# Kernel optimization log

Measured on AMD Instinct MI355X. Metric: run time of the kernel, lower is better.

## Reference

```python
import jax, jax.numpy as jnp
import numpy as np

B, S0, S1 = 4, 768, 256
T = S0 + S1
W0, W1 = 2048, 1024
N, K, H = 8, 1, 256  # num_heads, num_kv_heads (MQA), head_dim
G = N // K
MAX_WAVELENGTH = 10000.0
BIG_NEG = -2.3819763e+38


def _apply_rope(x, positions):
    """RoPE: positions [B,L] applied to x [B,L,heads,H]."""
    half = x.shape[-1] // 2
    freq_exponents = (2.0 / x.shape[-1]) * jnp.arange(half, dtype=jnp.float32)
    timescale = MAX_WAVELENGTH ** freq_exponents  # [half]
    radians = positions[..., None].astype(jnp.float32) / timescale  # [B,L,half]
    radians = radians[..., None, :]  # [B,L,1,half]
    sin, cos = jnp.sin(radians), jnp.cos(radians)
    x1, x2 = jnp.split(x.astype(jnp.float32), 2, axis=-1)
    res = jnp.concatenate([x1 * cos - x2 * sin, x2 * cos + x1 * sin], axis=-1)
    return res.astype(x.dtype)


def setup_inputs() -> dict:
    key = jax.random.key(0)
    ks = jax.random.split(key, 8)
    x0 = jax.random.normal(ks[0], (B, S0, W0), dtype=jnp.float32)
    x1 = jax.random.normal(ks[1], (B, S1, W1), dtype=jnp.float32)
    positions = jnp.broadcast_to(jnp.arange(T, dtype=jnp.int32)[None, :], (B, T))
    # causal mask [B,1,T,T]
    attn_mask = jnp.broadcast_to(jnp.tril(jnp.ones((T, T), dtype=bool))[None, None], (B, 1, T, T))
    # lecun_normal on the width (in) axis
    q0_w = jax.random.normal(ks[2], (N, W0, H), dtype=jnp.float32) / np.sqrt(W0)
    kv0_w = jax.random.normal(ks[3], (2, K, W0, H), dtype=jnp.float32) / np.sqrt(W0)
    out0_w = jax.random.normal(ks[4], (N, H, W0), dtype=jnp.float32) / np.sqrt(N * H)
    q1_w = jax.random.normal(ks[5], (N, W1, H), dtype=jnp.float32) / np.sqrt(W1)
    kv1_w = jax.random.normal(ks[6], (2, K, W1, H), dtype=jnp.float32) / np.sqrt(W1)
    out1_w = jax.random.normal(ks[7], (N, H, W1), dtype=jnp.float32) / np.sqrt(N * H)
    return {"x0": x0, "x1": x1, "positions": positions, "attn_mask": attn_mask,
            "q0_w": q0_w, "kv0_w": kv0_w, "out0_w": out0_w,
            "q1_w": q1_w, "kv1_w": kv1_w, "out1_w": out1_w}


def reference(x0, x1, positions, attn_mask, q0_w, kv0_w, out0_w, q1_w, kv1_w, out1_w):
    dtype = x0.dtype
    # per-modality QKV projections (num_kv_heads != num_heads branch)
    q0 = jnp.einsum('BTD,NDH->BTNH', x0, q0_w.astype(dtype))
    k0, v0 = jnp.einsum('BSD,2KDH->2BSKH', x0, kv0_w.astype(dtype))
    q1 = jnp.einsum('BTD,NDH->BTNH', x1, q1_w.astype(dtype))
    k1, v1 = jnp.einsum('BSD,2KDH->2BSKH', x1, kv1_w.astype(dtype))
    q = jnp.concatenate([q0, q1], axis=1)  # [B,T,N,H]
    k = jnp.concatenate([k0, k1], axis=1)  # [B,T,K,H]
    v = jnp.concatenate([v0, v1], axis=1)
    q = _apply_rope(q, positions) * (H ** -0.5)
    k = _apply_rope(k, positions)
    # prefill cache init: cache_size == attn_mask.shape[-1] == T, so no padding
    idx = jnp.full((B,), T, dtype=jnp.int32)
    # GQA attention
    qg = q.reshape(B, T, K, G, H)  # 'B T (K G) H -> B T K G H'
    logits = jnp.einsum('BTKGH,BSKH->BKGTS', qg, k, preferred_element_type=jnp.float32)
    masked = jnp.where(attn_mask[:, :, None, :, :], logits, BIG_NEG)
    probs = jax.nn.softmax(masked, axis=-1).astype(dtype)
    enc = jnp.einsum('BKGTS,BSKH->BTKGH', probs, v).reshape(B, T, N, H)
    out0 = jnp.einsum('BTNH,NHD->BTD', enc[:, :S0], out0_w.astype(dtype))
    out1 = jnp.einsum('BTNH,NHD->BTD', enc[:, S0:], out1_w.astype(dtype))
    return (out0, out1, idx, k, v)
```

## Files before the change

kernel.cpp:

```cpp
#include <hip/hip_runtime.h>

typedef unsigned short u16;
typedef __attribute__((ext_vector_type(8))) short short8;
typedef __attribute__((ext_vector_type(4))) float f32x4;
typedef __attribute__((ext_vector_type(4))) unsigned short u16x4;

__device__ __forceinline__ u16 f2bf(float f){
  unsigned u = __float_as_uint(f);
  u += 0x7FFFu + ((u >> 16) & 1u);
  return (u16)(u >> 16);
}
__device__ __forceinline__ float bf2f(u16 h){
  return __uint_as_float(((unsigned)h) << 16);
}
__device__ __forceinline__ void gload16(const void* g, void* l){
  __builtin_amdgcn_global_load_lds((const __attribute__((address_space(1))) void*)g,
                                   (__attribute__((address_space(3))) void*)l, 16, 0, 0);
}
__device__ __forceinline__ f32x4 mfma16(short8 a, short8 b, f32x4 c){
  return __builtin_amdgcn_mfma_f32_16x16x32_bf16(a, b, c, 0, 0, 0);
}
__device__ __forceinline__ short8 ld8(const u16* p){
  return *reinterpret_cast<const short8*>(p);
}

template<int CTRL>
__device__ __forceinline__ float dppf(float x){
  return __int_as_float(__builtin_amdgcn_update_dpp(0, __float_as_int(x), CTRL, 0xF, 0xF, true));
}
__device__ __forceinline__ float rmax16(float x){
  x = fmaxf(x, dppf<0xB1>(x));
  x = fmaxf(x, dppf<0x4E>(x));
  x = fmaxf(x, dppf<0x124>(x));
  x = fmaxf(x, dppf<0x128>(x));
  return x;
}
__device__ __forceinline__ float rsum16(float x){
  x += dppf<0xB1>(x);
  x += dppf<0x4E>(x);
  x += dppf<0x124>(x);
  x += dppf<0x128>(x);
  return x;
}

__global__ void cvt_all(const float* __restrict__ x0, const float* __restrict__ x1,
                        u16* __restrict__ x0b, u16* __restrict__ x1b){
  int bid = blockIdx.x;
  const float* s; u16* d; int i;
  if (bid < 6144){ s = x0; d = x0b; i = bid * 256 + threadIdx.x; }
  else           { s = x1; d = x1b; i = (bid - 6144) * 256 + threadIdx.x; }
  float4 v = reinterpret_cast<const float4*>(s)[i];
  u16x4 o = { f2bf(v.x), f2bf(v.y), f2bf(v.z), f2bf(v.w) };
  reinterpret_cast<u16x4*>(d)[i] = o;
}

__device__ __forceinline__
void transp_body(const float* __restrict__ S, u16* __restrict__ D,
                 int K, int C, int kb, int cb){
  __shared__ float t[32][33];
  int tx = threadIdx.x & 31, ty = threadIdx.x >> 5;
  #pragma unroll
  for (int i = ty; i < 32; i += 8)
    t[i][tx] = S[(size_t)(kb + i) * C + cb + tx];
  __syncthreads();
  #pragma unroll
  for (int i = ty; i < 32; i += 8)
    D[(size_t)(cb + i) * K + kb + tx] = f2bf(t[tx][i]);
}
__global__ __launch_bounds__(256)
void transpose_all(const float* q0_w, const float* kv0_w, const float* q1_w,
                   const float* kv1_w, const float* o0_w, const float* o1_w,
                   u16* qkv0T, u16* qkv1T, u16* o0T, u16* o1T){
  int bid = blockIdx.x;
  const float* S; u16* D; int K, C, nkc, lid;
  if (bid < 4096){
    S = q0_w; D = qkv0T; K = 2048; C = 256; lid = bid;
  } else if (bid < 5120){
    S = kv0_w; D = qkv0T + (size_t)2048*2048; K = 2048; C = 256; lid = bid - 4096;
  } else if (bid < 7168){
    S = q1_w; D = qkv1T; K = 1024; C = 256; lid = bid - 5120;
  } else if (bid < 7680){
    S = kv1_w; D = qkv1T + (size_t)2048*1024; K = 1024; C = 256; lid = bid - 7168;
  } else if (bid < 11776){
    S = o0_w; D = o0T; K = 2048; C = 2048; lid = bid - 7680;
  } else {
    S = o1_w; D = o1T; K = 2048; C = 1024; lid = bid - 11776;
  }
  nkc = (K >> 5) * (C >> 5);
  int z   = lid / nkc;
  int rem = lid - z * nkc;
  int kb  = (rem / (C >> 5)) << 5;
  int cb  = (rem % (C >> 5)) << 5;
  transp_body(S + (size_t)z * K * C, D + (size_t)z * K * C, K, C, kb, cb);
}

__device__ __forceinline__
void gemm_body(const u16* __restrict__ A, int lda, int aS, int aT, int aOff,
               const u16* __restrict__ BT, int ldbt,
               u16* __restrict__ Cb, float* __restrict__ Cf, int ldc,
               int cS, int cT, int cOff, int N, int Kd, int bid, char* smem){
  int ntx = N >> 7;
  int bm = bid / ntx;
  int bn = bid - bm * ntx;
  int row0 = bm << 7, col0 = bn << 7;
  size_t arow0 = (size_t)(row0 / aS) * aT + (row0 % aS) + aOff;
  size_t crow0 = (size_t)(row0 / cS) * cT + (row0 % cS) + cOff;
  const u16* Abase = A + arow0 * (size_t)lda;
  const u16* Bbase = BT + (size_t)col0 * ldbt;
  int tid = threadIdx.x;
  int w = tid >> 6, l = tid & 63;
  int wr = (w >> 1) << 6, wc = (w & 1) << 6;
  int lr = l & 15, g4 = l >> 4, lq = (l >> 4) << 2;
  int keyr = lr & 7;
  f32x4 acc[4][4];
  #pragma unroll
  for (int m = 0; m < 4; m++)
    #pragma unroll
    for (int n = 0; n < 4; n++)
      acc[m][n] = (f32x4){0.f, 0.f, 0.f, 0.f};
  int scol = (((tid & 7) ^ ((tid >> 3) & 7)) << 3);
  const u16* gA = Abase + (size_t)(tid >> 3) * lda + scol;
  const u16* gB = Bbase + (size_t)(tid >> 3) * ldbt + scol;
  int dsto = tid * 16;

  auto STAGE = [&](char* dst, int k0){
    gload16(gA + k0,                      dst + dsto);
    gload16(gA + (size_t)32*lda  + k0,    dst + 4096  + dsto);
    gload16(gA + (size_t)64*lda  + k0,    dst + 8192  + dsto);
    gload16(gA + (size_t)96*lda  + k0,    dst + 12288 + dsto);
    gload16(gB + k0,                      dst + 16384 + dsto);
    gload16(gB + (size_t)32*ldbt + k0,    dst + 20480 + dsto);
    gload16(gB + (size_t)64*ldbt + k0,    dst + 24576 + dsto);
    gload16(gB + (size_t)96*ldbt + k0,    dst + 28672 + dsto);
  };

  STAGE(smem, 0);
  int cur = 0;
  for (int k0 = 0; k0 < Kd; k0 += 64, cur ^= 1){
    asm volatile("" ::: "memory");
    __builtin_amdgcn_s_barrier();
    asm volatile("" ::: "memory");
    if (k0 + 64 < Kd){
      STAGE(smem + (cur ^ 1) * 32768, k0 + 64);
      asm volatile("s_waitcnt vmcnt(8)" ::: "memory");
    } else {
      asm volatile("s_waitcnt vmcnt(0)" ::: "memory");
    }
    __builtin_amdgcn_s_barrier();
    asm volatile("" ::: "memory");
    const u16* As = (const u16*)(smem + cur * 32768);
    const u16* Bs = As + 8192;
    #pragma unroll
    for (int kk = 0; kk < 2; kk++){
      int so = ((g4 + kk*4) ^ keyr) << 3;
      short8 af[4], bfr[4];
      #pragma unroll
      for (int m = 0; m < 4; m++)
        af[m] = ld8(&As[(wr + m*16 + lr)*64 + so]);
      #pragma unroll
      for (int n = 0; n < 4; n++)
        bfr[n] = ld8(&Bs[(wc + n*16 + lr)*64 + so]);
      #pragma unroll
      for (int m = 0; m < 4; m++)
        #pragma unroll
        for (int n = 0; n < 4; n++)
          acc[m][n] = mfma16(af[m], bfr[n], acc[m][n]);
    }
  }
  #pragma unroll
  for (int m = 0; m < 4; m++){
    #pragma unroll
    for (int i = 0; i < 4; i++){
      size_t r = crow0 + wr + m*16 + lq + i;
      if (Cb){
        #pragma unroll
        for (int n = 0; n < 4; n++)
          Cb[r*ldc + col0 + wc + n*16 + lr] = f2bf(acc[m][n][i]);
      } else {
        #pragma unroll
        for (int n = 0; n < 4; n++)
          Cf[r*ldc + col0 + wc + n*16 + lr] = acc[m][n][i];
      }
    }
  }
}

__global__ __launch_bounds__(256)
void gemm_qkv(const u16* __restrict__ x0b, const u16* __restrict__ qkv0T,
              const u16* __restrict__ x1b, const u16* __restrict__ qkv1T,
              u16* __restrict__ qkvb){
  extern __shared__ __align__(16) char smem[];
  int bid = blockIdx.x;
  if (bid < 480)
    gemm_body(x0b, 2048, 3072, 3072, 0, qkv0T, 2048,
              qkvb, nullptr, 2560, 768, 1024, 0, 2560, 2048, bid, smem);
  else
    gemm_body(x1b, 1024, 1024, 1024, 0, qkv1T, 1024,
              qkvb, nullptr, 2560, 256, 1024, 768, 2560, 1024, bid - 480, smem);
}

__global__ __launch_bounds__(256)
void gemm_out(const u16* __restrict__ encb, const u16* __restrict__ o0T,
              const u16* __restrict__ o1T, float* __restrict__ out0,
              float* __restrict__ out1){
  extern __shared__ __align__(16) char smem[];
  int bid = blockIdx.x;
  if (bid < 384)
    gemm_body(encb, 2048, 768, 1024, 0, o0T, 2048,
              nullptr, out0, 2048, 3072, 3072, 0, 2048, 2048, bid, smem);
  else
    gemm_body(encb, 2048, 256, 1024, 768, o1T, 2048,
              nullptr, out1, 1024, 1024, 1024, 0, 1024, 2048, bid - 384, smem);
}

__global__ void rope_kernel(u16* __restrict__ qkv, const int* __restrict__ positions,
                            float* __restrict__ k_out, float* __restrict__ v_out,
                            float* __restrict__ idx_out){
  int bt = blockIdx.x;
  int j = threadIdx.x;
  float pos = (float)positions[bt];
  float ts = powf(10000.0f, (float)j * 0.0078125f);
  float rad = pos / ts;
  float sn, cs;
  sincosf(rad, &sn, &cs);
  u16* q = qkv + (size_t)bt * 2560;
  #pragma unroll
  for (int n = 0; n < 8; n++){
    float x1 = bf2f(q[n*256 + j]);
    float x2 = bf2f(q[n*256 + 128 + j]);
    q[n*256 + j]       = f2bf((x1*cs - x2*sn) * 0.0625f);
    q[n*256 + 128 + j] = f2bf((x2*cs + x1*sn) * 0.0625f);
  }
  u16* kv = q + 2048;
  float x1 = bf2f(kv[j]), x2 = bf2f(kv[128 + j]);
  float k1 = x1*cs - x2*sn, k2 = x2*cs + x1*sn;
  kv[j] = f2bf(k1); kv[128 + j] = f2bf(k2);
  size_t ko = (size_t)bt * 256;
  k_out[ko + j] = k1;  k_out[ko + 128 + j] = k2;
  v_out[ko + j] = bf2f(kv[256 + j]);
  v_out[ko + 128 + j] = bf2f(kv[384 + j]);
  if (bt == 0 && j < 4) idx_out[j] = 1024.0f;
}

__global__ void transpose_v(const u16* __restrict__ qkv, u16* __restrict__ vT){
  __shared__ u16 t[32][33];
  int b = blockIdx.z;
  int tb = blockIdx.x * 32, hb = blockIdx.y * 32;
  int tx = threadIdx.x, ty = threadIdx.y;
  #pragma unroll
  for (int i = ty; i < 32; i += 8)
    t[i][tx] = qkv[(size_t)(b*1024 + tb + i)*2560 + 2304 + hb + tx];
  __syncthreads();
  #pragma unroll
  for (int i = ty; i < 32; i += 8)
    vT[(size_t)(b*256 + hb + i)*1024 + tb + tx] = t[tx][i];
}

__global__ __launch_bounds__(256, 2)
void attn_kernel(const u16* __restrict__ qkv, const u16* __restrict__ vT,
                 u16* __restrict__ enc){
  extern __shared__ __align__(16) char smem[];
  int bid = blockIdx.x;
  int b   = bid & 3;
  int h2  = (bid >> 2) & 1;
  int qt  = 63 - (bid >> 3);
  int tid = threadIdx.x;
  int w = tid >> 6;
  int head = h2*4 + w;
  int l = tid & 63;
  int lr = l & 15;
  int g4 = l >> 4;
  int lkqe  = g4 << 3;
  int lkq16 = g4 << 4;
  int lq = g4 << 2;
  int q0 = qt << 4, nkv = q0 + 16;
  int swk = (lr & 7) << 4;
  int swv = ((lr >> 1) & 3) << 4;
  int swp = ((lr >> 2) & 3) << 4;

  const char* kbase = (const char*)qkv + (size_t)b*5242880 + 4096;
  const char* vbase = (const char*)vT + (size_t)b*524288;
  const char* ksrc[4]; const char* vsrc[4];
  int kldo[4], vldo[4];
  #pragma unroll
  for (int r = 0; r < 4; r++){
    int o = r*4096 + tid*16;
    int krow = o >> 9;
    int kcol = (o & 511) ^ ((krow & 7) << 4);
    ksrc[r] = kbase + (size_t)krow*5120 + kcol;
    kldo[r] = o;
    int vrow = o >> 6;
    int vcol = (o & 63) ^ (((vrow >> 1) & 3) << 4);
    vsrc[r] = vbase + (size_t)vrow*2048 + vcol;
    vldo[r] = 16384 + o;
  }

  const u16* qb = qkv + ((size_t)(b*1024 + q0)) * 2560 + head*256;
  short8 qf[8];
  #pragma unroll
  for (int hf = 0; hf < 8; hf++)
    qf[hf] = ld8(qb + (size_t)lr*2560 + hf*32 + lkqe);

  f32x4 o_[16];
  #pragma unroll
  for (int hf = 0; hf < 16; hf++)
    o_[hf] = (f32x4){0.f,0.f,0.f,0.f};
  float mrow[4], lrow[4];
  #pragma unroll
  for (int i = 0; i < 4; i++){ mrow[i] = -3.0e38f; lrow[i] = 0.f; }
  u16* P = (u16*)(smem + 65536 + w*1024);

  auto STAGE = [&](int buf, int kt){
    char* dst = smem + buf*32768;
    #pragma unroll
    for (int r = 0; r < 4; r++)
      gload16(ksrc[r] + (size_t)kt*5120, dst + kldo[r]);
    #pragma unroll
    for (int r = 0; r < 4; r++)
      gload16(vsrc[r] + (size_t)kt*2, dst + vldo[r]);
  };

  STAGE(0, 0);
  int cur = 0;
  for (int kt = 0; kt < nkv; kt += 32, cur ^= 1){
    asm volatile("" ::: "memory");
    __builtin_amdgcn_s_barrier();
    asm volatile("" ::: "memory");
    if (kt + 32 < nkv){
      STAGE(cur ^ 1, kt + 32);
      asm volatile("s_waitcnt vmcnt(8)" ::: "memory");
    } else {
      asm volatile("s_waitcnt vmcnt(0)" ::: "memory");
    }
    __builtin_amdgcn_s_barrier();
    asm volatile("" ::: "memory");

    const char* Kb = smem + cur*32768;
    const char* Vb = Kb + 16384;
    f32x4 s[2];
    s[0] = (f32x4){0.f,0.f,0.f,0.f};
    s[1] = (f32x4){0.f,0.f,0.f,0.f};
    #pragma unroll
    for (int hf = 0; hf < 8; hf++){
      int colb = (hf*64 + lkq16) ^ swk;
      short8 k0 = *(const short8*)(Kb + (size_t)(lr     )*512 + colb);
      short8 k1 = *(const short8*)(Kb + (size_t)(lr + 16)*512 + colb);
      s[0] = mfma16(qf[hf], k0, s[0]);
      s[1] = mfma16(qf[hf], k1, s[1]);
    }
    if (kt + 32 > q0){
      #pragma unroll
      for (int cf = 0; cf < 2; cf++)
        #pragma unroll
        for (int i = 0; i < 4; i++){
          int row_g = q0 + lq + i;
          int col_g = kt + cf*16 + lr;
          if (col_g > row_g) s[cf][i] = -1.0e30f;
        }
    }
    float mx[4];
    #pragma unroll
    for (int i = 0; i < 4; i++)
      mx[i] = rmax16(fmaxf(s[0][i], s[1][i]));
    bool nd = false;
    #pragma unroll
    for (int i = 0; i < 4; i++)
      nd = nd || (mx[i] > mrow[i] + 8.f);
    if (__ballot(nd)){
      #pragma unroll
      for (int i = 0; i < 4; i++){
        float mn = fmaxf(mrow[i], mx[i]);
        float corr = __expf(mrow[i] - mn);
        mrow[i] = mn;
        lrow[i] *= corr;
        #pragma unroll
        for (int hf = 0; hf < 16; hf++)
          o_[hf][i] *= corr;
      }
    }
    #pragma unroll
    for (int i = 0; i < 4; i++){
      float m = mrow[i];
      float p0 = __expf(s[0][i] - m);
      float p1 = __expf(s[1][i] - m);
      s[0][i] = p0; s[1][i] = p1;
      lrow[i] += rsum16(p0 + p1);
    }
    asm volatile("s_waitcnt lgkmcnt(0)" ::: "memory");
    __builtin_amdgcn_sched_barrier(0);
    #pragma unroll
    for (int cf = 0; cf < 2; cf++)
      #pragma unroll
      for (int i = 0; i < 4; i++){
        int row = lq + i;
        int by = ((row*32 + cf*16 + lr) << 1) ^ (((row >> 2) & 3) << 4);
        *(u16*)((char*)P + by) = f2bf(s[cf][i]);
      }
    asm volatile("s_waitcnt lgkmcnt(0)" ::: "memory");
    __builtin_amdgcn_sched_barrier(0);
    short8 pa;
    {
      int by = ((lr*32 + lkqe) << 1) ^ swp;
      pa = *(const short8*)((const char*)P + by);
    }
    __builtin_amdgcn_sched_barrier(0);
    #pragma unroll
    for (int hf = 0; hf < 16; hf++){
      const char* vr = Vb + (size_t)(hf*16 + lr)*64;
      short8 v0 = *(const short8*)(vr + (lkq16 ^ swv));
      o_[hf] = mfma16(pa, v0, o_[hf]);
    }
  }
  u16* eb = enc + ((size_t)(b*1024 + q0)) * 2048 + head*256;
  float inv[4];
  #pragma unroll
  for (int i = 0; i < 4; i++)
    inv[i] = 1.0f / lrow[i];
  #pragma unroll
  for (int hf = 0; hf < 16; hf++)
    #pragma unroll
    for (int i = 0; i < 4; i++)
      eb[(size_t)(lq + i)*2048 + hf*16 + lr] = f2bf(o_[hf][i] * inv[i]);
}

extern "C" void kernel_launch(void* const* d_in, const int* in_sizes, int n_in,
                              void* d_out, int out_size, void* d_ws, size_t ws_size,
                              hipStream_t stream){
  const float* x0     = (const float*)d_in[0];
  const float* x1     = (const float*)d_in[1];
  const int*   pos    = (const int*)d_in[2];
  const float* q0_w   = (const float*)d_in[4];
  const float* kv0_w  = (const float*)d_in[5];
  const float* out0_w = (const float*)d_in[6];
  const float* q1_w   = (const float*)d_in[7];
  const float* kv1_w  = (const float*)d_in[8];
  const float* out1_w = (const float*)d_in[9];

  float* out  = (float*)d_out;
  float* out0 = out;
  float* out1 = out + 6291456;
  float* idxp = out + 7340032;
  float* kout = out + 7340036;
  float* vout = out + 8388612;

  char* ws = (char*)d_ws;
  size_t off = 0;
  auto alloc = [&](size_t bytes){
    void* p = ws + off;
    off = (off + bytes + 255) & ~(size_t)255;
    return p;
  };
  u16* x0b   = (u16*)alloc((size_t)6291456 * 2);
  u16* x1b   = (u16*)alloc((size_t)1048576 * 2);
  u16* qkv0T = (u16*)alloc((size_t)2560 * 2048 * 2);
  u16* qkv1T = (u16*)alloc((size_t)2560 * 1024 * 2);
  u16* o0T   = (u16*)alloc((size_t)2048 * 2048 * 2);
  u16* o1T   = (u16*)alloc((size_t)1024 * 2048 * 2);
  u16* qkvb  = (u16*)alloc((size_t)4096 * 2560 * 2);
  u16* vTb   = (u16*)alloc((size_t)4 * 256 * 1024 * 2);
  u16* encb  = (u16*)alloc((size_t)4096 * 2048 * 2);

  hipFuncSetAttribute((const void*)attn_kernel,
                      hipFuncAttributeMaxDynamicSharedMemorySize, 69632);
  hipFuncSetAttribute((const void*)gemm_qkv,
                      hipFuncAttributeMaxDynamicSharedMemorySize, 65536);
  hipFuncSetAttribute((const void*)gemm_out,
                      hipFuncAttributeMaxDynamicSharedMemorySize, 65536);

  cvt_all<<<7168, 256, 0, stream>>>(x0, x1, x0b, x1b);
  transpose_all<<<13824, 256, 0, stream>>>(q0_w, kv0_w, q1_w, kv1_w, out0_w, out1_w,
                                           qkv0T, qkv1T, o0T, o1T);

  gemm_qkv<<<640, 256, 65536, stream>>>(x0b, qkv0T, x1b, qkv1T, qkvb);

  rope_kernel<<<4096, 128, 0, stream>>>(qkvb, pos, kout, vout, idxp);
  transpose_v<<<dim3(32, 8, 4), dim3(32,8), 0, stream>>>(qkvb, vTb);
  attn_kernel<<<512, 256, 69632, stream>>>(qkvb, vTb, encb);

  gemm_out<<<448, 256, 65536, stream>>>(encb, o0T, o1T, out0, out1);
}
```

Measured before the change: 168.6 us.

## Transpose attention MFMA operands to keep P in registers and skip LDS

Swaps the A/B operands of the QK^T and PV MFMAs so each lane holds one query row's scores. Softmax reductions then shrink to two cross-lane shuffles instead of DPP row reductions. The P tile is packed to bf16 with v_cvt_pk and rearranged into the PV operand layout through lane shuffles, so the LDS round-trip and its waits go away and the LDS allocation shrinks. The MFMA sections are also wrapped in s_setprio, and output stores become 8-byte vector writes. The risk is extra shuffle and select work, plus getting the register permutation exactly right.

```diff
diff --git a/kernel.cpp b/kernel.cpp
--- a/kernel.cpp
+++ b/kernel.cpp
@@ -23,24 +23,10 @@
 __device__ __forceinline__ short8 ld8(const u16* p){
   return *reinterpret_cast<const short8*>(p);
 }
-
-template<int CTRL>
-__device__ __forceinline__ float dppf(float x){
-  return __int_as_float(__builtin_amdgcn_update_dpp(0, __float_as_int(x), CTRL, 0xF, 0xF, true));
-}
-__device__ __forceinline__ float rmax16(float x){
-  x = fmaxf(x, dppf<0xB1>(x));
-  x = fmaxf(x, dppf<0x4E>(x));
-  x = fmaxf(x, dppf<0x124>(x));
-  x = fmaxf(x, dppf<0x128>(x));
-  return x;
-}
-__device__ __forceinline__ float rsum16(float x){
-  x += dppf<0xB1>(x);
-  x += dppf<0x4E>(x);
-  x += dppf<0x124>(x);
-  x += dppf<0x128>(x);
-  return x;
+__device__ __forceinline__ unsigned cvtpk(float lo, float hi){
+  unsigned r;
+  asm volatile("v_cvt_pk_bf16_f32 %0, %1, %2" : "=v"(r) : "v"(lo), "v"(hi));
+  return r;
 }
 
 __global__ void cvt_all(const float* __restrict__ x0, const float* __restrict__ x1,
@@ -269,14 +255,12 @@
   int head = h2*4 + w;
   int l = tid & 63;
   int lr = l & 15;
-  int g4 = l >> 4;
-  int lkqe  = g4 << 3;
-  int lkq16 = g4 << 4;
-  int lq = g4 << 2;
+  int g = l >> 4;
+  int lkqe  = g << 3;
+  int lkq16 = g << 4;
   int q0 = qt << 4, nkv = q0 + 16;
   int swk = (lr & 7) << 4;
   int swv = ((lr >> 1) & 3) << 4;
-  int swp = ((lr >> 2) & 3) << 4;
 
   const char* kbase = (const char*)qkv + (size_t)b*5242880 + 4096;
   const char* vbase = (const char*)vT + (size_t)b*524288;
@@ -305,10 +289,7 @@
   #pragma unroll
   for (int hf = 0; hf < 16; hf++)
     o_[hf] = (f32x4){0.f,0.f,0.f,0.f};
-  float mrow[4], lrow[4];
-  #pragma unroll
-  for (int i = 0; i < 4; i++){ mrow[i] = -3.0e38f; lrow[i] = 0.f; }
-  u16* P = (u16*)(smem + 65536 + w*1024);
+  float mrow = -3.0e38f, lrow = 0.f;
 
   auto STAGE = [&](int buf, int kt){
     char* dst = smem + buf*32768;
@@ -340,87 +321,84 @@
     f32x4 s[2];
     s[0] = (f32x4){0.f,0.f,0.f,0.f};
     s[1] = (f32x4){0.f,0.f,0.f,0.f};
+    __builtin_amdgcn_s_setprio(1);
     #pragma unroll
     for (int hf = 0; hf < 8; hf++){
       int colb = (hf*64 + lkq16) ^ swk;
       short8 k0 = *(const short8*)(Kb + (size_t)(lr     )*512 + colb);
       short8 k1 = *(const short8*)(Kb + (size_t)(lr + 16)*512 + colb);
-      s[0] = mfma16(qf[hf], k0, s[0]);
-      s[1] = mfma16(qf[hf], k1, s[1]);
-    }
+      s[0] = mfma16(k0, qf[hf], s[0]);
+      s[1] = mfma16(k1, qf[hf], s[1]);
+    }
+    __builtin_amdgcn_s_setprio(0);
     if (kt + 32 > q0){
       #pragma unroll
       for (int cf = 0; cf < 2; cf++)
         #pragma unroll
         for (int i = 0; i < 4; i++){
-          int row_g = q0 + lq + i;
-          int col_g = kt + cf*16 + lr;
-          if (col_g > row_g) s[cf][i] = -1.0e30f;
+          int kv_g = kt + cf*16 + g*4 + i;
+          if (kv_g > q0 + lr) s[cf][i] = -1.0e30f;
         }
     }
-    float mx[4];
-    #pragma unroll
-    for (int i = 0; i < 4; i++)
-      mx[i] = rmax16(fmaxf(s[0][i], s[1][i]));
-    bool nd = false;
-    #pragma unroll
-    for (int i = 0; i < 4; i++)
-      nd = nd || (mx[i] > mrow[i] + 8.f);
+    float m8 = fmaxf(fmaxf(fmaxf(s[0][0], s[0][1]), fmaxf(s[0][2], s[0][3])),
+                     fmaxf(fmaxf(s[1][0], s[1][1]), fmaxf(s[1][2], s[1][3])));
+    m8 = fmaxf(m8, __shfl_xor(m8, 16, 64));
+    m8 = fmaxf(m8, __shfl_xor(m8, 32, 64));
+    bool nd = (m8 > mrow + 8.f);
     if (__ballot(nd)){
-      #pragma unroll
-      for (int i = 0; i < 4; i++){
-        float mn = fmaxf(mrow[i], mx[i]);
-        float corr = __expf(mrow[i] - mn);
-        mrow[i] = mn;
-        lrow[i] *= corr;
+      float mn = fmaxf(mrow, m8);
+      float corr = __expf(mrow - mn);
+      mrow = mn;
+      lrow *= corr;
+      #pragma unroll
+      for (int hf = 0; hf < 16; hf++)
         #pragma unroll
-        for (int hf = 0; hf < 16; hf++)
+        for (int i = 0; i < 4; i++)
           o_[hf][i] *= corr;
-      }
-    }
-    #pragma unroll
-    for (int i = 0; i < 4; i++){
-      float m = mrow[i];
-      float p0 = __expf(s[0][i] - m);
-      float p1 = __expf(s[1][i] - m);
-      s[0][i] = p0; s[1][i] = p1;
-      lrow[i] += rsum16(p0 + p1);
-    }
-    asm volatile("s_waitcnt lgkmcnt(0)" ::: "memory");
-    __builtin_amdgcn_sched_barrier(0);
+    }
+    float p[2][4];
     #pragma unroll
     for (int cf = 0; cf < 2; cf++)
       #pragma unroll
-      for (int i = 0; i < 4; i++){
-        int row = lq + i;
-        int by = ((row*32 + cf*16 + lr) << 1) ^ (((row >> 2) & 3) << 4);
-        *(u16*)((char*)P + by) = f2bf(s[cf][i]);
-      }
-    asm volatile("s_waitcnt lgkmcnt(0)" ::: "memory");
-    __builtin_amdgcn_sched_barrier(0);
-    short8 pa;
-    {
-      int by = ((lr*32 + lkqe) << 1) ^ swp;
-      pa = *(const short8*)((const char*)P + by);
-    }
-    __builtin_amdgcn_sched_barrier(0);
+      for (int i = 0; i < 4; i++)
+        p[cf][i] = __expf(s[cf][i] - mrow);
+    float sum8 = p[0][0] + p[0][1] + p[0][2] + p[0][3]
+               + p[1][0] + p[1][1] + p[1][2] + p[1][3];
+    sum8 += __shfl_xor(sum8, 16, 64);
+    sum8 += __shfl_xor(sum8, 32, 64);
+    lrow += sum8;
+    unsigned A0 = cvtpk(p[0][0], p[0][1]);
+    unsigned A1 = cvtpk(p[0][2], p[0][3]);
+    unsigned B0 = cvtpk(p[1][0], p[1][1]);
+    unsigned B1 = cvtpk(p[1][2], p[1][3]);
+    unsigned sp0 = (unsigned)__shfl_xor((int)(g < 2 ? A0 : B0), 16, 64);
+    unsigned sp1 = (unsigned)__shfl_xor((int)(g < 2 ? A1 : B1), 16, 64);
+    unsigned c0  = (unsigned)__shfl_xor((int)(l < 32 ? B0 : A0), 32, 64);
+    unsigned c1  = (unsigned)__shfl_xor((int)(l < 32 ? B1 : A1), 32, 64);
+    unsigned pc0 = (unsigned)__shfl_xor((int)c0, 16, 64);
+    unsigned pc1 = (unsigned)__shfl_xor((int)c1, 16, 64);
+    union { unsigned u[4]; short8 v; } pf;
+    pf.u[0] = (g == 0) ? A0 : (g == 1) ? pc0 : (g == 2) ? c0  : sp0;
+    pf.u[1] = (g == 0) ? A1 : (g == 1) ? pc1 : (g == 2) ? c1  : sp1;
+    pf.u[2] = (g == 0) ? sp0 : (g == 1) ? c0 : (g == 2) ? pc0 : B0;
+    pf.u[3] = (g == 0) ? sp1 : (g == 1) ? c1 : (g == 2) ? pc1 : B1;
+    __builtin_amdgcn_s_setprio(1);
     #pragma unroll
     for (int hf = 0; hf < 16; hf++){
       const char* vr = Vb + (size_t)(hf*16 + lr)*64;
       short8 v0 = *(const short8*)(vr + (lkq16 ^ swv));
-      o_[hf] = mfma16(pa, v0, o_[hf]);
-    }
-  }
-  u16* eb = enc + ((size_t)(b*1024 + q0)) * 2048 + head*256;
-  float inv[4];
-  #pragma unroll
-  for (int i = 0; i < 4; i++)
-    inv[i] = 1.0f / lrow[i];
-  #pragma unroll
-  for (int hf = 0; hf < 16; hf++)
-    #pragma unroll
-    for (int i = 0; i < 4; i++)
-      eb[(size_t)(lq + i)*2048 + hf*16 + lr] = f2bf(o_[hf][i] * inv[i]);
+      o_[hf] = mfma16(v0, pf.v, o_[hf]);
+    }
+    __builtin_amdgcn_s_setprio(0);
+  }
+  u16* eb = enc + ((size_t)(b*1024 + q0 + lr)) * 2048 + head*256;
+  float inv = 1.0f / lrow;
+  #pragma unroll
+  for (int hf = 0; hf < 16; hf++){
+    u16x4 st = { f2bf(o_[hf][0] * inv), f2bf(o_[hf][1] * inv),
+                 f2bf(o_[hf][2] * inv), f2bf(o_[hf][3] * inv) };
+    *reinterpret_cast<u16x4*>(eb + hf*16 + g*4) = st;
+  }
 }
 
 extern "C" void kernel_launch(void* const* d_in, const int* in_sizes, int n_in,
@@ -461,7 +439,7 @@
   u16* encb  = (u16*)alloc((size_t)4096 * 2048 * 2);
 
   hipFuncSetAttribute((const void*)attn_kernel,
-                      hipFuncAttributeMaxDynamicSharedMemorySize, 69632);
+                      hipFuncAttributeMaxDynamicSharedMemorySize, 65536);
   hipFuncSetAttribute((const void*)gemm_qkv,
                       hipFuncAttributeMaxDynamicSharedMemorySize, 65536);
   hipFuncSetAttribute((const void*)gemm_out,
@@ -475,7 +453,7 @@
 
   rope_kernel<<<4096, 128, 0, stream>>>(qkvb, pos, kout, vout, idxp);
   transpose_v<<<dim3(32, 8, 4), dim3(32,8), 0, stream>>>(qkvb, vTb);
-  attn_kernel<<<512, 256, 69632, stream>>>(qkvb, vTb, encb);
+  attn_kernel<<<512, 256, 65536, stream>>>(qkvb, vTb, encb);
 
   gemm_out<<<448, 256, 65536, stream>>>(encb, o0T, o1T, out0, out1);
 }
```

Result: no change. 168.0 us (-0.4%).
